# Kernel tuning notes

Hardware: AMD Instinct MI355X
Metric: run time of the kernel (lower is better)

The kernel has to match this reference:

```python
import jax, jax.numpy as jnp
import numpy as np

N = 100_000      # nodes
E = 1_000_000    # edges
F_IN = 32        # num_features
F_OUT = 32       # out_channels
K = 3            # num_filters (diffusion steps)


def setup_inputs() -> dict:
    key = jax.random.key(0)
    ks = jax.random.split(key, 12)
    d_in = F_IN + F_OUT  # gates see concat([X, H])
    s = 1.0 / np.sqrt(d_in)
    inp = {
        "x": jax.random.normal(ks[0], (N, F_IN), jnp.float32),
        "edge_index": jax.random.randint(ks[1], (2, E), 0, N, dtype=jnp.int32),
        "edge_weight": jax.random.uniform(ks[2], (E,), jnp.float32, 0.01, 1.0),
        "h": jnp.zeros((N, F_OUT), jnp.float32),
        "c": jnp.zeros((N, F_OUT), jnp.float32),
        # DConv weights: [2 directions, K hops, d_in, F_OUT] per gate
        "Wz": s * jax.random.normal(ks[3], (2, K, d_in, F_OUT), jnp.float32),
        "bz": jnp.zeros((F_OUT,), jnp.float32),
        "Wr": s * jax.random.normal(ks[4], (2, K, d_in, F_OUT), jnp.float32),
        "br": jnp.zeros((F_OUT,), jnp.float32),
        "Wh": s * jax.random.normal(ks[5], (2, K, d_in, F_OUT), jnp.float32),
        "bh": jnp.zeros((F_OUT,), jnp.float32),
        "Wl": s * jax.random.normal(ks[6], (F_OUT, 1), jnp.float32),
        "bl": jnp.zeros((1,), jnp.float32),
    }
    return inp


def _dconv(X, src, dst, ew, W, b):
    """Bidirectional K-hop diffusion conv (DCRNN DConv). X: [N, d_in]."""
    n = X.shape[0]
    deg_out = jax.ops.segment_sum(ew, src, num_segments=n)  # weighted out-degree
    deg_in = jax.ops.segment_sum(ew, dst, num_segments=n)   # weighted in-degree
    norm_out = ew / deg_out[src]  # D_out^{-1} W random walk
    norm_in = ew / deg_in[dst]    # D_in^{-1} W^T random walk

    def prop_out(v):  # forward diffusion: aggregate at dst from src
        return jax.ops.segment_sum(norm_out[:, None] * v[src], dst, num_segments=n)

    def prop_in(v):   # reverse diffusion: aggregate at src from dst
        return jax.ops.segment_sum(norm_in[:, None] * v[dst], src, num_segments=n)

    H = X @ W[0, 0] + X @ W[1, 0]
    Kk = W.shape[1]
    if Kk > 1:
        T0o = T0i = X
        T1o, T1i = prop_out(X), prop_in(X)
        H = H + T1o @ W[0, 1] + T1i @ W[1, 1]
        for k in range(2, Kk):
            T2o = 2.0 * prop_out(T1o) - T0o
            T2i = 2.0 * prop_in(T1i) - T0i
            H = H + T2o @ W[0, k] + T2i @ W[1, k]
            T0o, T1o = T1o, T2o
            T0i, T1i = T1i, T2i
    return H + b


def reference(x, edge_index, edge_weight, h, c, Wz, bz, Wr, br, Wh, bh, Wl, bl):
    src, dst = edge_index[0], edge_index[1]
    # wrapper passes H=None (h_1 = None) -> hidden state initialized to zeros
    H0 = jnp.zeros((x.shape[0], F_OUT), x.dtype)
    XH = jnp.concatenate([x, H0], axis=1)
    Z = jax.nn.sigmoid(_dconv(XH, src, dst, edge_weight, Wz, bz))
    R = jax.nn.sigmoid(_dconv(XH, src, dst, edge_weight, Wr, br))
    XRH = jnp.concatenate([x, R * H0], axis=1)
    H_tilde = jnp.tanh(_dconv(XRH, src, dst, edge_weight, Wh, bh))
    H = Z * H0 + (1.0 - Z) * H_tilde  # GRU update
    y = jax.nn.relu(H) @ Wl + bl      # relu + linear head
    return y
```

## Files before the change

kernel.cpp:

```cpp
#include <hip/hip_runtime.h>
#include <math.h>

#define NN 100000
#define NE 1000000
#define F 32
#define NBKT 196
#define BKT2 (2 * NBKT)
#define CAPB 5888
#define EB 4096
#define NTILE 6250

typedef unsigned short ushortT;
typedef unsigned int uintT;
typedef __attribute__((ext_vector_type(8))) short short8;
typedef __attribute__((ext_vector_type(4))) float f32x4;

__device__ inline float bfhi(uintT u)  { return __int_as_float(u & 0xffff0000u); }
__device__ inline float bflo(uintT u)  { return __int_as_float(u << 16); }
__device__ inline uintT f2bf(float f) {
    uintT u = __float_as_uint(f);
    return (u + 0x7fffu + ((u >> 16) & 1u)) >> 16;
}
__device__ inline uintT pack15(float f) {
    uintT u = __float_as_uint(f);
    return ((u + 0x7fffu + ((u >> 16) & 1u)) >> 16) & 0x7fffu;
}
__device__ inline float unpack15(uintT v) { return __int_as_float((v & 0x7fffu) << 16); }

__launch_bounds__(256)
__global__ void k_bucket(const int* __restrict__ ei, const float* __restrict__ ew,
                         int* __restrict__ cursor, uint2* __restrict__ stg) {
    __shared__ int se_s[EB];
    __shared__ int se_d[EB];
    __shared__ uintT se_w[EB];
    __shared__ int cntL[BKT2], baseL[BKT2], curL[BKT2];

    const int tid = threadIdx.x;
    const int e0  = blockIdx.x * EB;

    for (int b = tid; b < BKT2; b += 256) { cntL[b] = 0; curL[b] = 0; }
    __syncthreads();

#pragma unroll
    for (int k = 0; k < EB / 256; ++k) {
        int i = tid + k * 256;
        int gid = e0 + i;
        int s = -1, d = -1; uintT w = 0;
        if (gid < NE) {
            s = ei[gid]; d = ei[NE + gid]; w = pack15(ew[gid]);
            atomicAdd(&cntL[d >> 9], 1);
            atomicAdd(&cntL[NBKT + (s >> 9)], 1);
        }
        se_s[i] = s; se_d[i] = d; se_w[i] = w;
    }
    __syncthreads();

    for (int b = tid; b < BKT2; b += 256)
        if (cntL[b] > 0) baseL[b] = atomicAdd(&cursor[b], cntL[b]);
    __syncthreads();

#pragma unroll
    for (int k = 0; k < EB / 256; ++k) {
        int i = tid + k * 256;
        int s = se_s[i];
        if (s < 0) continue;
        int d = se_d[i]; uintT w = se_w[i];
        int b0 = d >> 9;
        int p0 = baseL[b0] + atomicAdd(&curL[b0], 1);
        if (p0 < CAPB) stg[(size_t)b0 * CAPB + p0] = make_uint2(((uintT)s << 15) | w, (uintT)(d & 511));
        int b1 = NBKT + (s >> 9);
        int p1 = baseL[b1] + atomicAdd(&curL[b1], 1);
        if (p1 < CAPB) stg[(size_t)b1 * CAPB + p1] = make_uint2(((uintT)d << 15) | w, (uintT)(s & 511));
    }
}

__launch_bounds__(256)
__global__ void k_csr(const int* __restrict__ cursor, const uint2* __restrict__ stg,
                      uintT* __restrict__ entF, int2* __restrict__ meta,
                      float* __restrict__ rdeg) {
    __shared__ int   ncnt[512];
    __shared__ int   nbase[512];
    __shared__ int   ncur[512];
    __shared__ float wsum[512];
    __shared__ int   wavesum[4];

    const int b   = blockIdx.x;
    const int tid = threadIdx.x;
    const int dir = (b >= NBKT) ? 1 : 0;
    const int n0  = (dir ? (b - NBKT) : b) << 9;
    const int c   = min(cursor[b], CAPB);
    const uint2* S = stg + (size_t)b * CAPB;

    for (int l = tid; l < 512; l += 256) { ncnt[l] = 0; ncur[l] = 0; wsum[l] = 0.f; }
    __syncthreads();

    for (int i = tid; i < c; i += 256) {
        uint2 it = S[i];
        atomicAdd(&ncnt[it.y], 1);
        atomicAdd(&wsum[it.y], unpack15(it.x));
    }
    __syncthreads();

    int v0 = ncnt[2 * tid], v1 = ncnt[2 * tid + 1];
    int sp = v0 + v1;
    int lane = tid & 63, wid = tid >> 6;
    int incl = sp;
#pragma unroll
    for (int o = 1; o < 64; o <<= 1) {
        int t = __shfl_up(incl, o, 64);
        if (lane >= o) incl += t;
    }
    if (lane == 63) wavesum[wid] = incl;
    __syncthreads();
    int woff = 0;
    for (int wq = 0; wq < wid; ++wq) woff += wavesum[wq];
    int ex = incl - sp + woff;
    nbase[2 * tid] = ex;
    nbase[2 * tid + 1] = ex + v0;
    __syncthreads();

    const int rb = b * CAPB;
    for (int l = tid; l < 512; l += 256) {
        int node = n0 + l;
        if (node < NN) {
            int seg = dir * NN + node;
            meta[seg] = make_int2(rb + nbase[l], ncnt[l]);
            float s = wsum[l];
            rdeg[seg] = 1.0f / ((s > 0.f) ? s : 1.0f);
        }
    }
    __syncthreads();

    for (int i = tid; i < c; i += 256) {
        uint2 it = S[i];
        int r = atomicAdd(&ncur[it.y], 1);
        entF[rb + nbase[it.y] + r] = it.x;
    }
}

__global__ void k_wprep(const float* __restrict__ Wz, const float* __restrict__ Wh,
                        ushortT* __restrict__ wfrag) {
    int gid = blockIdx.x * 256 + threadIdx.x;
    if (gid >= 20 * 512) return;
    int f = gid >> 9, rem = gid & 511;
    int l = rem >> 3, r = rem & 7;
    int kc = f >> 2, nt = f & 3;
    int n = nt * 16 + (l & 15);
    int fi = (l >> 4) * 8 + r;
    int jc = n & 31;
    const float* W = (n >= 32) ? Wh : Wz;
#define WDK(d, k) W[((((d) * 3 + (k)) * 64) + fi) * 32 + jc]
    float v;
    if      (kc == 0) v = WDK(0,0) + WDK(1,0) - WDK(0,2) - WDK(1,2);
    else if (kc == 1) v = WDK(0,1);
    else if (kc == 2) v = WDK(1,1);
    else if (kc == 3) v = 2.0f * WDK(0,2);
    else              v = 2.0f * WDK(1,2);
#undef WDK
    wfrag[gid] = (ushortT)f2bf(v);
}

__global__ void k_conv(const float* __restrict__ x, ushortT* __restrict__ xbr) {
    int i = blockIdx.x * 256 + threadIdx.x;
    if (i >= NN * F / 8) return;
    const float4* p = (const float4*)x + (long)i * 2;
    float4 a = p[0], b = p[1];
    uint4 o;
    o.x = f2bf(a.x) | (f2bf(a.y) << 16);
    o.y = f2bf(a.z) | (f2bf(a.w) << 16);
    o.z = f2bf(b.x) | (f2bf(b.y) << 16);
    o.w = f2bf(b.z) | (f2bf(b.w) << 16);
    ((uint4*)xbr)[i] = o;
}

__launch_bounds__(256)
__global__ void k_hop(const int2* __restrict__ meta, const uintT* __restrict__ entF,
                      const float* __restrict__ rdeg,
                      const ushortT* __restrict__ fo, const ushortT* __restrict__ fi,
                      ushortT* __restrict__ oo, ushortT* __restrict__ oi) {
    const int dir = blockIdx.x & 1;
    const int n   = (blockIdx.x >> 1) * 32 + (threadIdx.x >> 3);
    if (n >= NN) return;
    const int q   = threadIdx.x & 7;
    const int2 m  = meta[dir * NN + n];
    const int opp = dir ? 0 : NN;
    const ushortT* __restrict__ feat = dir ? fi : fo;

    float ax = 0.f, ay = 0.f, az = 0.f, aw = 0.f;
    const int end = m.x + m.y;
    int p = m.x;
    for (; p + 8 <= end; p += 8) {
        float nms[8]; uint2 vs[8];
#pragma unroll
        for (int k = 0; k < 8; ++k) {
            uintT en = entF[p + k];
            int idx = (int)(en >> 15);
            nms[k] = unpack15(en) * rdeg[opp + idx];
            vs[k]  = *(const uint2*)(feat + (long)idx * F + q * 4);
        }
#pragma unroll
        for (int k = 0; k < 8; ++k) {
            ax += nms[k] * bflo(vs[k].x);
            ay += nms[k] * bfhi(vs[k].x);
            az += nms[k] * bflo(vs[k].y);
            aw += nms[k] * bfhi(vs[k].y);
        }
    }
    for (; p < end; ++p) {
        uintT en = entF[p];
        int idx = (int)(en >> 15);
        float nm = unpack15(en) * rdeg[opp + idx];
        uint2 v = *(const uint2*)(feat + (long)idx * F + q * 4);
        ax += nm * bflo(v.x);
        ay += nm * bfhi(v.x);
        az += nm * bflo(v.y);
        aw += nm * bfhi(v.y);
    }
    uint2 o = make_uint2(f2bf(ax) | (f2bf(ay) << 16), f2bf(az) | (f2bf(aw) << 16));
    *(uint2*)((dir ? oi : oo) + (long)n * F + q * 4) = o;
}

__launch_bounds__(256)
__global__ void k_final(const ushortT* __restrict__ xb,
                        const ushortT* __restrict__ t1o, const ushortT* __restrict__ t1i,
                        const ushortT* __restrict__ p2o, const ushortT* __restrict__ p2i,
                        const ushortT* __restrict__ wfrag,
                        const float* __restrict__ bz, const float* __restrict__ bh,
                        const float* __restrict__ Wl, const float* __restrict__ bl,
                        float* __restrict__ y, int nwaves) {
    const int lane = threadIdx.x & 63;
    const int wgid = blockIdx.x * 4 + (threadIdx.x >> 6);
    const int quad = lane >> 4;
    const int c0   = lane & 15;

    union U8 { uint4 u; short8 s; };

    short8 bfr[20];
#pragma unroll
    for (int f = 0; f < 20; ++f) {
        U8 t; t.u = *(const uint4*)(wfrag + f * 512 + lane * 8);
        bfr[f] = t.s;
    }

    const float bz0 = bz[c0], bz1 = bz[c0 + 16];
    const float bh0 = bh[c0], bh1 = bh[c0 + 16];
    const float wl0 = Wl[c0], wl1 = Wl[c0 + 16];
    const float blv = bl[0];

    const ushortT* srcs[5] = {xb, t1o, t1i, p2o, p2i};

    for (int t = wgid; t < NTILE; t += nwaves) {
        const long off = (long)t * 16 * F + (long)c0 * F + quad * 8;
        f32x4 a0 = {0.f, 0.f, 0.f, 0.f}, a1 = a0, a2 = a0, a3 = a0;
#pragma unroll
        for (int kc = 0; kc < 5; ++kc) {
            U8 av; av.u = *(const uint4*)(srcs[kc] + off);
            a0 = __builtin_amdgcn_mfma_f32_16x16x32_bf16(av.s, bfr[kc * 4 + 0], a0, 0, 0, 0);
            a1 = __builtin_amdgcn_mfma_f32_16x16x32_bf16(av.s, bfr[kc * 4 + 1], a1, 0, 0, 0);
            a2 = __builtin_amdgcn_mfma_f32_16x16x32_bf16(av.s, bfr[kc * 4 + 2], a2, 0, 0, 0);
            a3 = __builtin_amdgcn_mfma_f32_16x16x32_bf16(av.s, bfr[kc * 4 + 3], a3, 0, 0, 0);
        }
        float res[4];
#pragma unroll
        for (int r = 0; r < 4; ++r) {
            float gz = a0[r] + bz0, gh = a2[r] + bh0;
            float z  = 1.0f / (1.0f + __expf(-gz));
            float e2 = __expf(2.0f * gh);
            float ht = 1.0f - 2.0f / (e2 + 1.0f);
            float v  = fmaxf((1.0f - z) * ht, 0.0f) * wl0;
            gz = a1[r] + bz1; gh = a3[r] + bh1;
            z  = 1.0f / (1.0f + __expf(-gz));
            e2 = __expf(2.0f * gh);
            ht = 1.0f - 2.0f / (e2 + 1.0f);
            v += fmaxf((1.0f - z) * ht, 0.0f) * wl1;
            res[r] = v;
        }
#pragma unroll
        for (int o = 1; o < 16; o <<= 1) {
            res[0] += __shfl_xor(res[0], o, 64);
            res[1] += __shfl_xor(res[1], o, 64);
            res[2] += __shfl_xor(res[2], o, 64);
            res[3] += __shfl_xor(res[3], o, 64);
        }
        if (c0 == 0) {
            f32x4 out = {res[0] + blv, res[1] + blv, res[2] + blv, res[3] + blv};
            *(f32x4*)(y + t * 16 + quad * 4) = out;
        }
    }
}

extern "C" void kernel_launch(void* const* d_in, const int* in_sizes, int n_in,
                              void* d_out, int out_size, void* d_ws, size_t ws_size,
                              hipStream_t stream) {
    const float* x  = (const float*)d_in[0];
    const int*   ei = (const int*)  d_in[1];
    const float* ew = (const float*)d_in[2];
    const float* Wz = (const float*)d_in[5];
    const float* bz = (const float*)d_in[6];
    const float* Wh = (const float*)d_in[9];
    const float* bh = (const float*)d_in[10];
    const float* Wl = (const float*)d_in[11];
    const float* bl = (const float*)d_in[12];
    float* y = (float*)d_out;

    const size_t segs = 2 * NN;
    const long   NFW  = (long)NN * F;
    int*     cursor = (int*)d_ws;
    int2*    meta   = (int2*)(cursor + 400);
    float*   rdeg   = (float*)(meta + segs);
    uintT*   entF   = (uintT*)(rdeg + segs);
    ushortT* wfrag  = (ushortT*)(entF + (size_t)BKT2 * CAPB);
    ushortT* xbr    = wfrag + 10240;
    ushortT* t1o    = xbr + NFW;
    ushortT* t1i    = t1o + NFW;
    ushortT* p2o    = t1i + NFW;
    ushortT* p2i    = p2o + NFW;
    uint2*   stg    = (uint2*)t1o;

    hipMemsetAsync(cursor, 0, BKT2 * sizeof(int), stream);

    const int B = 256;
    k_conv<<<(NN * F / 8 + B - 1) / B, B, 0, stream>>>(x, xbr);
    k_wprep<<<40, B, 0, stream>>>(Wz, Wh, wfrag);
    k_bucket<<<(NE + EB - 1) / EB, B, 0, stream>>>(ei, ew, cursor, stg);
    k_csr<<<BKT2, B, 0, stream>>>(cursor, stg, entF, meta, rdeg);
    k_hop<<<2 * ((NN + 31) / 32), B, 0, stream>>>(meta, entF, rdeg, xbr, xbr, t1o, t1i);
    k_hop<<<2 * ((NN + 31) / 32), B, 0, stream>>>(meta, entF, rdeg, t1o, t1i, p2o, p2i);
    const int fblocks = 512;
    k_final<<<fblocks, B, 0, stream>>>(xbr, t1o, t1i, p2o, p2i, wfrag,
                                       bz, bh, Wl, bl, y, fblocks * 4);
}
```

Before: 237.5 us.

## Merge prep kernels, keep bucket edges in registers, predicate hop tail loop

The bf16 conversion of x and the weight-fragment prep are merged into one launch to save a kernel launch. k_bucket keeps its 16 edges per thread in registers instead of 48KB of shared memory, which raises occupancy. k_hop replaces the scalar remainder loop with a clamped, masked 8-wide batch so the tail gathers are issued together, at the cost of redundant loads for padded slots.

```diff
diff --git a/kernel.cpp b/kernel.cpp
--- a/kernel.cpp
+++ b/kernel.cpp
@@ -9,6 +9,7 @@
 #define CAPB 5888
 #define EB 4096
 #define NTILE 6250
+#define CONVB 1563
 
 typedef unsigned short ushortT;
 typedef unsigned int uintT;
@@ -30,9 +31,6 @@
 __launch_bounds__(256)
 __global__ void k_bucket(const int* __restrict__ ei, const float* __restrict__ ew,
                          int* __restrict__ cursor, uint2* __restrict__ stg) {
-    __shared__ int se_s[EB];
-    __shared__ int se_d[EB];
-    __shared__ uintT se_w[EB];
     __shared__ int cntL[BKT2], baseL[BKT2], curL[BKT2];
 
     const int tid = threadIdx.x;
@@ -41,17 +39,19 @@
     for (int b = tid; b < BKT2; b += 256) { cntL[b] = 0; curL[b] = 0; }
     __syncthreads();
 
+    int   rs[EB / 256];
+    int   rd[EB / 256];
+    uintT rw[EB / 256];
 #pragma unroll
     for (int k = 0; k < EB / 256; ++k) {
-        int i = tid + k * 256;
-        int gid = e0 + i;
+        int gid = e0 + tid + k * 256;
         int s = -1, d = -1; uintT w = 0;
         if (gid < NE) {
             s = ei[gid]; d = ei[NE + gid]; w = pack15(ew[gid]);
             atomicAdd(&cntL[d >> 9], 1);
             atomicAdd(&cntL[NBKT + (s >> 9)], 1);
         }
-        se_s[i] = s; se_d[i] = d; se_w[i] = w;
+        rs[k] = s; rd[k] = d; rw[k] = w;
     }
     __syncthreads();
 
@@ -61,10 +61,9 @@
 
 #pragma unroll
     for (int k = 0; k < EB / 256; ++k) {
-        int i = tid + k * 256;
-        int s = se_s[i];
+        int s = rs[k];
         if (s < 0) continue;
-        int d = se_d[i]; uintT w = se_w[i];
+        int d = rd[k]; uintT w = rw[k];
         int b0 = d >> 9;
         int p0 = baseL[b0] + atomicAdd(&curL[b0], 1);
         if (p0 < CAPB) stg[(size_t)b0 * CAPB + p0] = make_uint2(((uintT)s << 15) | w, (uintT)(d & 511));
@@ -138,9 +137,24 @@
     }
 }
 
-__global__ void k_wprep(const float* __restrict__ Wz, const float* __restrict__ Wh,
-                        ushortT* __restrict__ wfrag) {
-    int gid = blockIdx.x * 256 + threadIdx.x;
+__launch_bounds__(256)
+__global__ void k_prep(const float* __restrict__ x, ushortT* __restrict__ xbr,
+                       const float* __restrict__ Wz, const float* __restrict__ Wh,
+                       ushortT* __restrict__ wfrag) {
+    if (blockIdx.x < CONVB) {
+        int i = blockIdx.x * 256 + threadIdx.x;
+        if (i >= NN * F / 8) return;
+        const float4* p = (const float4*)x + (long)i * 2;
+        float4 a = p[0], b = p[1];
+        uint4 o;
+        o.x = f2bf(a.x) | (f2bf(a.y) << 16);
+        o.y = f2bf(a.z) | (f2bf(a.w) << 16);
+        o.z = f2bf(b.x) | (f2bf(b.y) << 16);
+        o.w = f2bf(b.z) | (f2bf(b.w) << 16);
+        ((uint4*)xbr)[i] = o;
+        return;
+    }
+    int gid = (blockIdx.x - CONVB) * 256 + threadIdx.x;
     if (gid >= 20 * 512) return;
     int f = gid >> 9, rem = gid & 511;
     int l = rem >> 3, r = rem & 7;
@@ -160,19 +174,6 @@
     wfrag[gid] = (ushortT)f2bf(v);
 }
 
-__global__ void k_conv(const float* __restrict__ x, ushortT* __restrict__ xbr) {
-    int i = blockIdx.x * 256 + threadIdx.x;
-    if (i >= NN * F / 8) return;
-    const float4* p = (const float4*)x + (long)i * 2;
-    float4 a = p[0], b = p[1];
-    uint4 o;
-    o.x = f2bf(a.x) | (f2bf(a.y) << 16);
-    o.y = f2bf(a.z) | (f2bf(a.w) << 16);
-    o.z = f2bf(b.x) | (f2bf(b.y) << 16);
-    o.w = f2bf(b.z) | (f2bf(b.w) << 16);
-    ((uint4*)xbr)[i] = o;
-}
-
 __launch_bounds__(256)
 __global__ void k_hop(const int2* __restrict__ meta, const uintT* __restrict__ entF,
                       const float* __restrict__ rdeg,
@@ -187,16 +188,18 @@
     const ushortT* __restrict__ feat = dir ? fi : fo;
 
     float ax = 0.f, ay = 0.f, az = 0.f, aw = 0.f;
-    const int end = m.x + m.y;
-    int p = m.x;
-    for (; p + 8 <= end; p += 8) {
+    const int end = m.x + m.y, last = end - 1;
+    for (int p = m.x; p < end; p += 8) {
         float nms[8]; uint2 vs[8];
 #pragma unroll
         for (int k = 0; k < 8; ++k) {
-            uintT en = entF[p + k];
+            int i  = p + k;
+            int ic = min(i, last);
+            uintT en = entF[ic];
             int idx = (int)(en >> 15);
-            nms[k] = unpack15(en) * rdeg[opp + idx];
+            float nm = unpack15(en) * rdeg[opp + idx];
             vs[k]  = *(const uint2*)(feat + (long)idx * F + q * 4);
+            nms[k] = (i < end) ? nm : 0.f;
         }
 #pragma unroll
         for (int k = 0; k < 8; ++k) {
@@ -205,16 +208,6 @@
             az += nms[k] * bflo(vs[k].y);
             aw += nms[k] * bfhi(vs[k].y);
         }
-    }
-    for (; p < end; ++p) {
-        uintT en = entF[p];
-        int idx = (int)(en >> 15);
-        float nm = unpack15(en) * rdeg[opp + idx];
-        uint2 v = *(const uint2*)(feat + (long)idx * F + q * 4);
-        ax += nm * bflo(v.x);
-        ay += nm * bfhi(v.x);
-        az += nm * bflo(v.y);
-        aw += nm * bfhi(v.y);
     }
     uint2 o = make_uint2(f2bf(ax) | (f2bf(ay) << 16), f2bf(az) | (f2bf(aw) << 16));
     *(uint2*)((dir ? oi : oo) + (long)n * F + q * 4) = o;
@@ -320,8 +313,7 @@
     hipMemsetAsync(cursor, 0, BKT2 * sizeof(int), stream);
 
     const int B = 256;
-    k_conv<<<(NN * F / 8 + B - 1) / B, B, 0, stream>>>(x, xbr);
-    k_wprep<<<40, B, 0, stream>>>(Wz, Wh, wfrag);
+    k_prep<<<CONVB + 40, B, 0, stream>>>(x, xbr, Wz, Wh, wfrag);
     k_bucket<<<(NE + EB - 1) / EB, B, 0, stream>>>(ei, ew, cursor, stg);
     k_csr<<<BKT2, B, 0, stream>>>(cursor, stg, entF, meta, rdeg);
     k_hop<<<2 * ((NN + 31) / 32), B, 0, stream>>>(meta, entF, rdeg, xbr, xbr, t1o, t1i);
```

Result: faster. 224.4 us (-5.5%).
